# Optimization experiments

Measured on AMD Instinct MI355X. Metric: run time of the kernel, lower is better.

Reference implementation:

```python
import jax, jax.numpy as jnp
import numpy as np

N_NODES = 81
N_EDGES = 1620
IN_DIM = 10
HIDDEN = 8192
ACTIONS = 729


def setup_inputs() -> dict:
    key = jax.random.key(0)
    ks = jax.random.split(key, 8)
    x = jax.random.normal(ks[0], (N_NODES, IN_DIM), dtype=jnp.float32)
    edge_index = jax.random.randint(ks[1], (2, N_EDGES), 0, N_NODES, dtype=jnp.int64)
    W_gcn = jax.random.normal(ks[2], (IN_DIM, HIDDEN), dtype=jnp.float32) / np.sqrt(IN_DIM)
    b_gcn = jnp.zeros((HIDDEN,), dtype=jnp.float32)
    ln_g = jnp.ones((HIDDEN,), dtype=jnp.float32)
    ln_b = jnp.zeros((HIDDEN,), dtype=jnp.float32)
    W1 = jax.random.normal(ks[3], (HIDDEN, HIDDEN), dtype=jnp.float32) / np.sqrt(HIDDEN)
    b1 = jnp.zeros((HIDDEN,), dtype=jnp.float32)
    W2 = jax.random.normal(ks[4], (HIDDEN, ACTIONS), dtype=jnp.float32) / np.sqrt(HIDDEN)
    b2 = jnp.zeros((ACTIONS,), dtype=jnp.float32)
    return {"x": x, "edge_index": edge_index, "W_gcn": W_gcn, "b_gcn": b_gcn,
            "ln_g": ln_g, "ln_b": ln_b, "W1": W1, "b1": b1, "W2": W2, "b2": b2}


def _gcn_conv(x, edge_index, W, b):
    # GCNConv with added self-loops and symmetric D^-1/2 (A+I) D^-1/2 normalization
    n = x.shape[0]
    loops = jnp.arange(n, dtype=edge_index.dtype)
    src = jnp.concatenate([edge_index[0], loops])  # [E+N]
    dst = jnp.concatenate([edge_index[1], loops])
    h = x @ W  # [N, H] — transform before propagate, as in PyG
    deg = jnp.zeros((n,), dtype=h.dtype).at[dst].add(1.0)
    dinv = jnp.where(deg > 0, jax.lax.rsqrt(deg), 0.0)
    norm = dinv[src] * dinv[dst]  # [E+N]
    msg = h[src] * norm[:, None]
    out = jnp.zeros_like(h).at[dst].add(msg)
    return out + b


def _layer_norm(h, g, b, eps=1e-5):
    mu = jnp.mean(h, axis=-1, keepdims=True)
    var = jnp.mean(jnp.square(h - mu), axis=-1, keepdims=True)
    return (h - mu) * jax.lax.rsqrt(var + eps) * g + b


def reference(x, edge_index, W_gcn, b_gcn, ln_g, ln_b, W1, b1, W2, b2):
    h = jax.nn.relu(_gcn_conv(x, edge_index, W_gcn, b_gcn))  # [81, H]
    h = _layer_norm(h, ln_g, ln_b)
    # global_add_pool with batch = zeros(81): sum all nodes into one graph row
    g = jnp.sum(h, axis=0, keepdims=True)  # [1, H]
    g = jax.nn.relu(g @ W1 + b1)
    logits = g @ W2 + b2  # [1, ACTIONS]
    return jax.nn.log_softmax(logits, axis=1)
```

## Files before the change

### kernel.cpp

```cpp
#include <hip/hip_runtime.h>
#include <math.h>

#define N_NODES 81
#define N_EDGES 1620
#define IN_DIM 10
#define HIDDEN 8192
#define ACTIONS 729

__global__ __launch_bounds__(256) void stats_kernel(const float* __restrict__ x,
                                                    const int* __restrict__ ei,
                                                    const float* __restrict__ Wg,
                                                    const float* __restrict__ bg,
                                                    float* __restrict__ yr_all,
                                                    float* __restrict__ stats,
                                                    float* __restrict__ logits) {
    const int n = blockIdx.x;
    const int t = threadIdx.x;
    __shared__ float deg[N_NODES];
    __shared__ float yr[IN_DIM];
    __shared__ float red[8];

    if (t < N_NODES) deg[t] = 1.0f;
    if (t < IN_DIM) yr[t] = 0.0f;
    __syncthreads();
    for (int e = t; e < N_EDGES; e += 256) atomicAdd(&deg[ei[N_EDGES + e]], 1.0f);
    __syncthreads();
    if (t < N_NODES) deg[t] = rsqrtf(deg[t]);
    __syncthreads();
    const float dn = deg[n];
    for (int e = t; e < N_EDGES; e += 256) {
        if (ei[N_EDGES + e] == n) {
            int s = ei[e];
            float nrm = deg[s] * dn;
            #pragma unroll
            for (int c = 0; c < IN_DIM; ++c) atomicAdd(&yr[c], nrm * x[s * IN_DIM + c]);
        }
    }
    if (t == 0) {
        float nrm = dn * dn;
        #pragma unroll
        for (int c = 0; c < IN_DIM; ++c) atomicAdd(&yr[c], nrm * x[n * IN_DIM + c]);
    }
    __syncthreads();
    if (t < IN_DIM) yr_all[n * IN_DIM + t] = yr[t];
    if (n == 0) for (int a = t; a < ACTIONS; a += 256) logits[a] = 0.f;

    float s = 0.f, s2 = 0.f;
    #pragma unroll 4
    for (int k = 0; k < 32; ++k) {
        int j = t + k * 256;
        float h = bg[j];
        #pragma unroll
        for (int c = 0; c < IN_DIM; ++c) h = fmaf(yr[c], Wg[c * HIDDEN + j], h);
        h = fmaxf(h, 0.f);
        s += h; s2 += h * h;
    }
    #pragma unroll
    for (int off = 32; off > 0; off >>= 1) { s += __shfl_xor(s, off); s2 += __shfl_xor(s2, off); }
    int wave = t >> 6, lane = t & 63;
    if (lane == 0) { red[wave] = s; red[4 + wave] = s2; }
    __syncthreads();
    if (t == 0) {
        float S  = red[0] + red[1] + red[2] + red[3];
        float S2 = red[4] + red[5] + red[6] + red[7];
        float mu = S * (1.f / HIDDEN);
        float var = S2 * (1.f / HIDDEN) - mu * mu;
        stats[2 * n]     = mu;
        stats[2 * n + 1] = rsqrtf(var + 1e-5f);
    }
}

__global__ __launch_bounds__(256) void gemv1_kernel(const float* __restrict__ Wg,
                                                    const float* __restrict__ bg,
                                                    const float* __restrict__ lng,
                                                    const float* __restrict__ lnb,
                                                    const float* __restrict__ yr_all,
                                                    const float* __restrict__ stats,
                                                    const float* __restrict__ W1,
                                                    float* __restrict__ partial) {
    const int ct = blockIdx.x;
    const int ch = blockIdx.y;
    const int row0 = ch * 64;
    const int t = threadIdx.x;

    __shared__ float syr[N_NODES * IN_DIM];
    __shared__ float sstat[2 * N_NODES];
    __shared__ float sw[IN_DIM][64];
    __shared__ float gred[4][64];
    __shared__ float gl[64];

    for (int i = t; i < N_NODES * IN_DIM; i += 256) syr[i] = yr_all[i];
    for (int i = t; i < 2 * N_NODES; i += 256) sstat[i] = stats[i];
    if (t < 64) {
        #pragma unroll
        for (int c = 0; c < IN_DIM; ++c) sw[c][t] = Wg[c * HIDDEN + row0 + t];
    }
    __syncthreads();

    {
        const int r = t & 63, grp = t >> 6;
        const float bgv = bg[row0 + r];
        float acc = 0.f;
        for (int n = grp; n < N_NODES; n += 4) {
            float h = bgv;
            #pragma unroll
            for (int c = 0; c < IN_DIM; ++c) h = fmaf(syr[n * IN_DIM + c], sw[c][r], h);
            h = fmaxf(h, 0.f);
            acc += (h - sstat[2 * n]) * sstat[2 * n + 1];
        }
        gred[grp][r] = acc;
    }
    __syncthreads();
    if (t < 64)
        gl[t] = (gred[0][t] + gred[1][t] + gred[2][t] + gred[3][t]) * lng[row0 + t]
                + (float)N_NODES * lnb[row0 + t];
    __syncthreads();

    float4 acc = make_float4(0.f, 0.f, 0.f, 0.f);
    const float4* p = (const float4*)(W1 + (size_t)row0 * HIDDEN + ct * 1024) + t;
    #pragma unroll 8
    for (int i = 0; i < 64; ++i) {
        float4 w = p[(size_t)i * (HIDDEN / 4)];
        float gi = gl[i];
        acc.x = fmaf(gi, w.x, acc.x);
        acc.y = fmaf(gi, w.y, acc.y);
        acc.z = fmaf(gi, w.z, acc.z);
        acc.w = fmaf(gi, w.w, acc.w);
    }
    ((float4*)(partial + (size_t)ch * HIDDEN + ct * 1024))[t] = acc;
}

__global__ __launch_bounds__(256) void gemv2_kernel(const float* __restrict__ partial,
                                                    const float* __restrict__ b1,
                                                    const float* __restrict__ W2,
                                                    float* __restrict__ logits) {
    const int ch = blockIdx.x;
    const int row0 = ch * 32;
    const int t = threadIdx.x;
    __shared__ float sred[8][32];
    __shared__ float gl[32];

    {
        const int r = t & 31, grp = t >> 5;
        float a = 0.f;
        #pragma unroll 4
        for (int c = grp; c < 128; c += 8) a += partial[(size_t)c * HIDDEN + row0 + r];
        sred[grp][r] = a;
    }
    __syncthreads();
    if (t < 32) {
        float S = b1[row0 + t];
        #pragma unroll
        for (int gq = 0; gq < 8; ++gq) S += sred[gq][t];
        gl[t] = fmaxf(S, 0.f);
    }
    __syncthreads();

    float s0 = 0.f, s1 = 0.f, s2v = 0.f;
    const bool has2 = (t + 512) < ACTIONS;
    #pragma unroll 4
    for (int i = 0; i < 32; ++i) {
        float gi = gl[i];
        const float* r = W2 + (size_t)(row0 + i) * ACTIONS;
        s0 = fmaf(gi, r[t], s0);
        s1 = fmaf(gi, r[t + 256], s1);
        if (has2) s2v = fmaf(gi, r[t + 512], s2v);
    }
    atomicAdd(&logits[t], s0);
    atomicAdd(&logits[t + 256], s1);
    if (has2) atomicAdd(&logits[t + 512], s2v);
}

__global__ __launch_bounds__(256) void logsoftmax_kernel(const float* __restrict__ logits,
                                                         const float* __restrict__ b2,
                                                         float* __restrict__ out) {
    __shared__ float red[4];
    const int t = threadIdx.x;
    const bool has2 = (t + 512) < ACTIONS;
    float l0 = logits[t] + b2[t];
    float l1 = logits[t + 256] + b2[t + 256];
    float l2 = has2 ? (logits[t + 512] + b2[t + 512]) : -INFINITY;
    float m = fmaxf(fmaxf(l0, l1), l2);
    #pragma unroll
    for (int off = 32; off > 0; off >>= 1) m = fmaxf(m, __shfl_xor(m, off));
    int wave = t >> 6, lane = t & 63;
    if (lane == 0) red[wave] = m;
    __syncthreads();
    float M = fmaxf(fmaxf(red[0], red[1]), fmaxf(red[2], red[3]));
    __syncthreads();
    float e = __expf(l0 - M) + __expf(l1 - M) + (has2 ? __expf(l2 - M) : 0.f);
    #pragma unroll
    for (int off = 32; off > 0; off >>= 1) e += __shfl_xor(e, off);
    if (lane == 0) red[wave] = e;
    __syncthreads();
    float S = red[0] + red[1] + red[2] + red[3];
    float L = logf(S);
    out[t] = l0 - M - L;
    out[t + 256] = l1 - M - L;
    if (has2) out[t + 512] = l2 - M - L;
}

extern "C" void kernel_launch(void* const* d_in, const int* in_sizes, int n_in,
                              void* d_out, int out_size, void* d_ws, size_t ws_size,
                              hipStream_t stream) {
    const float* x    = (const float*)d_in[0];
    const int*   ei   = (const int*)  d_in[1];
    const float* Wg   = (const float*)d_in[2];
    const float* bg   = (const float*)d_in[3];
    const float* lng  = (const float*)d_in[4];
    const float* lnb  = (const float*)d_in[5];
    const float* W1   = (const float*)d_in[6];
    const float* b1   = (const float*)d_in[7];
    const float* W2   = (const float*)d_in[8];
    const float* b2   = (const float*)d_in[9];
    float* out = (float*)d_out;

    float* ws = (float*)d_ws;
    float* logits  = ws;
    float* stats   = ws + 1024;
    float* yr_all  = ws + 1280;
    float* partial = ws + 4096;

    stats_kernel<<<N_NODES, 256, 0, stream>>>(x, ei, Wg, bg, yr_all, stats, logits);
    gemv1_kernel<<<dim3(8, 128), 256, 0, stream>>>(Wg, bg, lng, lnb, yr_all, stats, W1, partial);
    gemv2_kernel<<<256, 256, 0, stream>>>(partial, b1, W2, logits);
    logsoftmax_kernel<<<1, 256, 0, stream>>>(logits, b2, out);
}
```

Baseline: 97.23 us.

## Materialize normalized node features and fuse log-softmax into last gemv2 block

The first kernel now writes the full normalized hidden matrix (81x8192) to workspace, so gemv1 sums precomputed values instead of recomputing the GCN projection per block from Wg, yr and the stats. The separate log-softmax launch is removed: gemv2 uses an atomic completion counter so the last finishing block computes the log-softmax. This trades redundant recomputation across 1024 gemv1 blocks for about 2.6 MB of extra global writes and reads, and saves one kernel launch at the cost of a threadfence and counter atomic in every gemv2 block.

```diff
diff --git a/kernel.cpp b/kernel.cpp
--- a/kernel.cpp
+++ b/kernel.cpp
@@ -7,13 +7,13 @@
 #define HIDDEN 8192
 #define ACTIONS 729
 
-__global__ __launch_bounds__(256) void stats_kernel(const float* __restrict__ x,
-                                                    const int* __restrict__ ei,
-                                                    const float* __restrict__ Wg,
-                                                    const float* __restrict__ bg,
-                                                    float* __restrict__ yr_all,
-                                                    float* __restrict__ stats,
-                                                    float* __restrict__ logits) {
+__global__ __launch_bounds__(256) void k1_kernel(const float* __restrict__ x,
+                                                 const int* __restrict__ ei,
+                                                 const float* __restrict__ Wg,
+                                                 const float* __restrict__ bg,
+                                                 float* __restrict__ hn,
+                                                 float* __restrict__ logits,
+                                                 unsigned* __restrict__ counter) {
     const int n = blockIdx.x;
     const int t = threadIdx.x;
     __shared__ float deg[N_NODES];
@@ -42,9 +42,12 @@
         for (int c = 0; c < IN_DIM; ++c) atomicAdd(&yr[c], nrm * x[n * IN_DIM + c]);
     }
     __syncthreads();
-    if (t < IN_DIM) yr_all[n * IN_DIM + t] = yr[t];
-    if (n == 0) for (int a = t; a < ACTIONS; a += 256) logits[a] = 0.f;
-
+    if (n == 0) {
+        for (int a = t; a < ACTIONS; a += 256) logits[a] = 0.f;
+        if (t == 0) *counter = 0u;
+    }
+
+    float vals[32];
     float s = 0.f, s2 = 0.f;
     #pragma unroll 4
     for (int k = 0; k < 32; ++k) {
@@ -53,6 +56,7 @@
         #pragma unroll
         for (int c = 0; c < IN_DIM; ++c) h = fmaf(yr[c], Wg[c * HIDDEN + j], h);
         h = fmaxf(h, 0.f);
+        vals[k] = h;
         s += h; s2 += h * h;
     }
     #pragma unroll
@@ -60,22 +64,21 @@
     int wave = t >> 6, lane = t & 63;
     if (lane == 0) { red[wave] = s; red[4 + wave] = s2; }
     __syncthreads();
-    if (t == 0) {
-        float S  = red[0] + red[1] + red[2] + red[3];
-        float S2 = red[4] + red[5] + red[6] + red[7];
-        float mu = S * (1.f / HIDDEN);
-        float var = S2 * (1.f / HIDDEN) - mu * mu;
-        stats[2 * n]     = mu;
-        stats[2 * n + 1] = rsqrtf(var + 1e-5f);
-    }
-}
-
-__global__ __launch_bounds__(256) void gemv1_kernel(const float* __restrict__ Wg,
-                                                    const float* __restrict__ bg,
+    float S  = red[0] + red[1] + red[2] + red[3];
+    float S2 = red[4] + red[5] + red[6] + red[7];
+    float mu = S * (1.f / HIDDEN);
+    float var = S2 * (1.f / HIDDEN) - mu * mu;
+    float inv = rsqrtf(var + 1e-5f);
+    #pragma unroll 4
+    for (int k = 0; k < 32; ++k) {
+        int j = t + k * 256;
+        hn[(size_t)n * HIDDEN + j] = (vals[k] - mu) * inv;
+    }
+}
+
+__global__ __launch_bounds__(256) void gemv1_kernel(const float* __restrict__ hn,
                                                     const float* __restrict__ lng,
                                                     const float* __restrict__ lnb,
-                                                    const float* __restrict__ yr_all,
-                                                    const float* __restrict__ stats,
                                                     const float* __restrict__ W1,
                                                     float* __restrict__ partial) {
     const int ct = blockIdx.x;
@@ -83,31 +86,14 @@
     const int row0 = ch * 64;
     const int t = threadIdx.x;
 
-    __shared__ float syr[N_NODES * IN_DIM];
-    __shared__ float sstat[2 * N_NODES];
-    __shared__ float sw[IN_DIM][64];
     __shared__ float gred[4][64];
     __shared__ float gl[64];
 
-    for (int i = t; i < N_NODES * IN_DIM; i += 256) syr[i] = yr_all[i];
-    for (int i = t; i < 2 * N_NODES; i += 256) sstat[i] = stats[i];
-    if (t < 64) {
-        #pragma unroll
-        for (int c = 0; c < IN_DIM; ++c) sw[c][t] = Wg[c * HIDDEN + row0 + t];
-    }
-    __syncthreads();
-
     {
         const int r = t & 63, grp = t >> 6;
-        const float bgv = bg[row0 + r];
         float acc = 0.f;
-        for (int n = grp; n < N_NODES; n += 4) {
-            float h = bgv;
-            #pragma unroll
-            for (int c = 0; c < IN_DIM; ++c) h = fmaf(syr[n * IN_DIM + c], sw[c][r], h);
-            h = fmaxf(h, 0.f);
-            acc += (h - sstat[2 * n]) * sstat[2 * n + 1];
-        }
+        for (int n = grp; n < N_NODES; n += 4)
+            acc += hn[(size_t)n * HIDDEN + row0 + r];
         gred[grp][r] = acc;
     }
     __syncthreads();
@@ -133,12 +119,16 @@
 __global__ __launch_bounds__(256) void gemv2_kernel(const float* __restrict__ partial,
                                                     const float* __restrict__ b1,
                                                     const float* __restrict__ W2,
-                                                    float* __restrict__ logits) {
+                                                    const float* __restrict__ b2,
+                                                    float* __restrict__ logits,
+                                                    unsigned* __restrict__ counter,
+                                                    float* __restrict__ out) {
     const int ch = blockIdx.x;
     const int row0 = ch * 32;
     const int t = threadIdx.x;
     __shared__ float sred[8][32];
     __shared__ float gl[32];
+    __shared__ int isLast;
 
     {
         const int r = t & 31, grp = t >> 5;
@@ -169,35 +159,34 @@
     atomicAdd(&logits[t], s0);
     atomicAdd(&logits[t + 256], s1);
     if (has2) atomicAdd(&logits[t + 512], s2v);
-}
-
-__global__ __launch_bounds__(256) void logsoftmax_kernel(const float* __restrict__ logits,
-                                                         const float* __restrict__ b2,
-                                                         float* __restrict__ out) {
-    __shared__ float red[4];
-    const int t = threadIdx.x;
-    const bool has2 = (t + 512) < ACTIONS;
-    float l0 = logits[t] + b2[t];
-    float l1 = logits[t + 256] + b2[t + 256];
-    float l2 = has2 ? (logits[t + 512] + b2[t + 512]) : -INFINITY;
-    float m = fmaxf(fmaxf(l0, l1), l2);
-    #pragma unroll
-    for (int off = 32; off > 0; off >>= 1) m = fmaxf(m, __shfl_xor(m, off));
-    int wave = t >> 6, lane = t & 63;
-    if (lane == 0) red[wave] = m;
-    __syncthreads();
-    float M = fmaxf(fmaxf(red[0], red[1]), fmaxf(red[2], red[3]));
-    __syncthreads();
-    float e = __expf(l0 - M) + __expf(l1 - M) + (has2 ? __expf(l2 - M) : 0.f);
-    #pragma unroll
-    for (int off = 32; off > 0; off >>= 1) e += __shfl_xor(e, off);
-    if (lane == 0) red[wave] = e;
-    __syncthreads();
-    float S = red[0] + red[1] + red[2] + red[3];
-    float L = logf(S);
-    out[t] = l0 - M - L;
-    out[t + 256] = l1 - M - L;
-    if (has2) out[t + 512] = l2 - M - L;
+
+    __threadfence();
+    __syncthreads();
+    if (t == 0) isLast = (atomicAdd(counter, 1u) == 255u) ? 1 : 0;
+    __syncthreads();
+    if (isLast) {
+        __threadfence();
+        float l0 = atomicAdd(&logits[t], 0.f) + b2[t];
+        float l1 = atomicAdd(&logits[t + 256], 0.f) + b2[t + 256];
+        float l2 = has2 ? (atomicAdd(&logits[t + 512], 0.f) + b2[t + 512]) : -INFINITY;
+        float m = fmaxf(fmaxf(l0, l1), l2);
+        #pragma unroll
+        for (int off = 32; off > 0; off >>= 1) m = fmaxf(m, __shfl_xor(m, off));
+        if ((t & 63) == 0) sred[0][t >> 6] = m;
+        __syncthreads();
+        float M = fmaxf(fmaxf(sred[0][0], sred[0][1]), fmaxf(sred[0][2], sred[0][3]));
+        __syncthreads();
+        float e = __expf(l0 - M) + __expf(l1 - M) + (has2 ? __expf(l2 - M) : 0.f);
+        #pragma unroll
+        for (int off = 32; off > 0; off >>= 1) e += __shfl_xor(e, off);
+        if ((t & 63) == 0) sred[0][t >> 6] = e;
+        __syncthreads();
+        float Se = sred[0][0] + sred[0][1] + sred[0][2] + sred[0][3];
+        float L = logf(Se);
+        out[t] = l0 - M - L;
+        out[t + 256] = l1 - M - L;
+        if (has2) out[t + 512] = l2 - M - L;
+    }
 }
 
 extern "C" void kernel_launch(void* const* d_in, const int* in_sizes, int n_in,
@@ -216,13 +205,12 @@
     float* out = (float*)d_out;
 
     float* ws = (float*)d_ws;
-    float* logits  = ws;
-    float* stats   = ws + 1024;
-    float* yr_all  = ws + 1280;
-    float* partial = ws + 4096;
-
-    stats_kernel<<<N_NODES, 256, 0, stream>>>(x, ei, Wg, bg, yr_all, stats, logits);
-    gemv1_kernel<<<dim3(8, 128), 256, 0, stream>>>(Wg, bg, lng, lnb, yr_all, stats, W1, partial);
-    gemv2_kernel<<<256, 256, 0, stream>>>(partial, b1, W2, logits);
-    logsoftmax_kernel<<<1, 256, 0, stream>>>(logits, b2, out);
-}
+    float* logits    = ws;
+    unsigned* counter = (unsigned*)(ws + 1024);
+    float* hn        = ws + 2048;
+    float* partial   = ws + 2048 + 663552;
+
+    k1_kernel<<<N_NODES, 256, 0, stream>>>(x, ei, Wg, bg, hn, logits, counter);
+    gemv1_kernel<<<dim3(8, 128), 256, 0, stream>>>(hn, lng, lnb, W1, partial);
+    gemv2_kernel<<<256, 256, 0, stream>>>(partial, b1, W2, b2, logits, counter, out);
+}
```

Result: slower. 124.6 us (+28.1%).
